# Kernel tuning notes

Hardware: AMD Instinct MI355X
Metric: run time of the kernel (lower is better)

The kernel has to match this reference:

```python
import jax, jax.numpy as jnp
import numpy as np

INPUT_SIZE = 300
HIDDEN = 128
NUM_CLASSES = 2
B, T = 256, 512


def setup_inputs() -> dict:
    key = jax.random.key(0)
    ks = jax.random.split(key, 7)
    s_ih = 1.0 / np.sqrt(HIDDEN)
    x = jax.random.normal(ks[0], (B, T, INPUT_SIZE), dtype=jnp.float32)
    W_ih = jax.random.uniform(ks[1], (HIDDEN, INPUT_SIZE), minval=-s_ih, maxval=s_ih, dtype=jnp.float32)
    W_hh = jax.random.uniform(ks[2], (HIDDEN, HIDDEN), minval=-s_ih, maxval=s_ih, dtype=jnp.float32)
    b_ih = jax.random.uniform(ks[3], (HIDDEN,), minval=-s_ih, maxval=s_ih, dtype=jnp.float32)
    b_hh = jax.random.uniform(ks[4], (HIDDEN,), minval=-s_ih, maxval=s_ih, dtype=jnp.float32)
    fc_w = jax.random.uniform(ks[5], (NUM_CLASSES, HIDDEN), minval=-s_ih, maxval=s_ih, dtype=jnp.float32)
    fc_b = jax.random.uniform(ks[6], (NUM_CLASSES,), minval=-s_ih, maxval=s_ih, dtype=jnp.float32)
    return {"x": x, "W_ih": W_ih, "W_hh": W_hh, "b_ih": b_ih, "b_hh": b_hh, "fc_w": fc_w, "fc_b": fc_b}


def reference(x, W_ih, W_hh, b_ih, b_hh, fc_w, fc_b):
    # Precompute input projections for all timesteps: [B,T,H]
    xp = jnp.einsum('bti,hi->bth', x, W_ih) + b_ih + b_hh
    h0 = jnp.zeros((x.shape[0], HIDDEN), dtype=x.dtype)

    def step(h, xp_t):  # xp_t: [B,H]
        h_new = jnp.tanh(xp_t + h @ W_hh.T)
        return h_new, None

    h_last, _ = jax.lax.scan(step, h0, jnp.swapaxes(xp, 0, 1))  # scan over T
    # Final FC on last hidden state (out[:, -1, :] of the RNN outputs)
    return h_last @ fc_w.T + fc_b
```

## Files before the change

kernel.cpp:

```cpp
#include <hip/hip_runtime.h>
#include <cstdint>
#include <cstddef>

#define KIN 300
#define KPAD 320
#define HIDDEN 128
#define BSZ 256
#define TSZ 512

typedef __attribute__((ext_vector_type(8))) short short8;
typedef __attribute__((ext_vector_type(4))) float f32x4;

__device__ __forceinline__ short f2bf(float f) {
  uint32_t u = __builtin_bit_cast(uint32_t, f);
  u = (u + 0x7FFFu + ((u >> 16) & 1u)) >> 16;
  return (short)u;
}
__device__ __forceinline__ float bf2f(short s) {
  uint32_t u = ((uint32_t)(uint16_t)s) << 16;
  return __builtin_bit_cast(float, u);
}
__device__ __forceinline__ float bflo(uint32_t u) {
  return __builtin_bit_cast(float, u << 16);
}
__device__ __forceinline__ float bfhi(uint32_t u) {
  return __builtin_bit_cast(float, u & 0xFFFF0000u);
}
__device__ __forceinline__ uint32_t pack2bf(float a, float b) {
  return (uint32_t)(uint16_t)f2bf(a) | ((uint32_t)(uint16_t)f2bf(b) << 16);
}
__device__ __forceinline__ float tanhf_fast(float v) {
  const float e = __builtin_amdgcn_exp2f(v * 2.88539008177793f);
  return fmaf(-2.0f, __builtin_amdgcn_rcpf(e + 1.0f), 1.0f);
}
__device__ __forceinline__ void barrier_lds() {
  asm volatile("s_waitcnt lgkmcnt(0)\n\ts_barrier" ::: "memory");
}
__device__ __forceinline__ void barrier_all() {
  asm volatile("s_waitcnt vmcnt(0) lgkmcnt(0)\n\ts_barrier" ::: "memory");
}
__device__ __forceinline__ void dma16(const short* g, short* l) {
  __builtin_amdgcn_global_load_lds(
      (const __attribute__((address_space(1))) void*)g,
      (__attribute__((address_space(3))) void*)l, 16, 0, 0);
}

__global__ __launch_bounds__(256) void wcvt_bf16(const float* __restrict__ W,
                                                 short* __restrict__ W16) {
  const int i = blockIdx.x * 256 + threadIdx.x;
  if (i >= HIDDEN * KPAD) return;
  const int n = i / KPAD, k = i % KPAD;
  W16[i] = (k < KIN) ? f2bf(W[n * KIN + k]) : (short)0;
}

__global__ __launch_bounds__(256) void xp_gemm_mfma(
    const float* __restrict__ x, const short* __restrict__ W16,
    const float* __restrict__ b_ih, const float* __restrict__ b_hh,
    short* __restrict__ xp16) {
  __shared__ __align__(16) short As[64 * 328];
  const int tid = threadIdx.x;
  const int lane = tid & 63, w = tid >> 6;
  const int q = lane >> 4, c = lane & 15;
  const int bg = blockIdx.x & 15, tc = blockIdx.x >> 4;
  const int b0 = bg * 16, t0 = tc * 4;

#pragma unroll
  for (int i = 0; i < 19; ++i) {
    const int f = tid + 256 * i;
    if (f < 4800) {
      const int rr = f / 75;
      const int k4 = f - rr * 75;
      const int b_in = rr >> 2, t_loc = rr & 3;
      const float4 v = *(const float4*)(
          x + ((size_t)(b0 + b_in) * TSZ + t0 + t_loc) * KIN + k4 * 4);
      uint2 pv;
      pv.x = pack2bf(v.x, v.y);
      pv.y = pack2bf(v.z, v.w);
      *(uint2*)&As[rr * 328 + k4 * 4] = pv;
    }
  }
  if (tid < 64) {
    const uint2 z = {0u, 0u};
#pragma unroll
    for (int j = 0; j < 5; ++j) *(uint2*)&As[tid * 328 + 300 + j * 4] = z;
  }
  __syncthreads();

  f32x4 acc[2][4];
#pragma unroll
  for (int ht = 0; ht < 2; ++ht)
#pragma unroll
    for (int rt = 0; rt < 4; ++rt) acc[ht][rt] = (f32x4){0.f, 0.f, 0.f, 0.f};

  const short* wp0 = W16 + (size_t)((2 * w + 0) * 16 + c) * KPAD + q * 8;
  const short* wp1 = W16 + (size_t)((2 * w + 1) * 16 + c) * KPAD + q * 8;
  short8 af[2][2];
  af[0][0] = *(const short8*)(wp0);
  af[0][1] = *(const short8*)(wp1);
#pragma unroll
  for (int kc = 0; kc < 10; ++kc) {
    const int cur = kc & 1;
    if (kc < 9) {
      af[cur ^ 1][0] = *(const short8*)(wp0 + (kc + 1) * 32);
      af[cur ^ 1][1] = *(const short8*)(wp1 + (kc + 1) * 32);
    }
    short8 bq[4];
#pragma unroll
    for (int rt = 0; rt < 4; ++rt)
      bq[rt] = *(const short8*)&As[(rt * 16 + c) * 328 + kc * 32 + q * 8];
#pragma unroll
    for (int ht = 0; ht < 2; ++ht)
#pragma unroll
      for (int rt = 0; rt < 4; ++rt)
        acc[ht][rt] = __builtin_amdgcn_mfma_f32_16x16x32_bf16(
            af[cur][ht], bq[rt], acc[ht][rt], 0, 0, 0);
  }
  __syncthreads();

  float4 bsum[2];
#pragma unroll
  for (int ht = 0; ht < 2; ++ht) {
    const int h0 = (2 * w + ht) * 16 + q * 4;
    const float4 bi = *(const float4*)(b_ih + h0);
    const float4 bh = *(const float4*)(b_hh + h0);
    bsum[ht] = make_float4(bi.x + bh.x, bi.y + bh.y, bi.z + bh.z, bi.w + bh.w);
  }
#pragma unroll
  for (int ht = 0; ht < 2; ++ht) {
    const int g = (2 * w + ht) * 4 + q;
#pragma unroll
    for (int rt = 0; rt < 4; ++rt) {
      const int b_in = rt * 4 + (c >> 2);
      const int t_loc = c & 3;
      uint2 pv;
      pv.x = pack2bf(acc[ht][rt][0] + bsum[ht].x, acc[ht][rt][1] + bsum[ht].y);
      pv.y = pack2bf(acc[ht][rt][2] + bsum[ht].z, acc[ht][rt][3] + bsum[ht].w);
      *(uint2*)&As[t_loc * 2312 + g * 72 + b_in * 4] = pv;
    }
  }
  __syncthreads();
#pragma unroll
  for (int i = 0; i < 4; ++i) {
    const int4 vv =
        *(const int4*)&As[i * 2312 + (tid >> 3) * 72 + (tid & 7) * 8];
    *(int4*)(xp16 + ((size_t)(t0 + i) * 16 + bg) * 2048 + tid * 8) = vv;
  }
}

__global__ __launch_bounds__(256, 1) void rnn_scan_dma(
    const short* __restrict__ xp16, const float* __restrict__ Whh,
    const float* __restrict__ fc_w, const float* __restrict__ fc_b,
    float* __restrict__ out) {
  __shared__ __align__(16) short xs[2][8][2048];
  __shared__ __align__(16) short ht[2][16][136];
  const int tid = threadIdx.x;
  const int lane = tid & 63, w = tid >> 6;
  const int q = lane >> 4, c = lane & 15;
  const int bg = blockIdx.x;

  short8 aw[2][4];
#pragma unroll
  for (int ti = 0; ti < 2; ++ti)
#pragma unroll
    for (int kc = 0; kc < 4; ++kc) {
      const float* src =
          Whh + (size_t)(w * 32 + ti * 16 + c) * HIDDEN + kc * 32 + q * 8;
      const float4 v0 = *(const float4*)(src);
      const float4 v1 = *(const float4*)(src + 4);
      short8 t;
      t[0] = f2bf(v0.x); t[1] = f2bf(v0.y); t[2] = f2bf(v0.z); t[3] = f2bf(v0.w);
      t[4] = f2bf(v1.x); t[5] = f2bf(v1.y); t[6] = f2bf(v1.z); t[7] = f2bf(v1.w);
      aw[ti][kc] = t;
    }

  {
    uint32_t* z = (uint32_t*)&ht[0][0][0];
    for (int i = tid; i < 1088; i += 256) z[i] = 0;
  }

#define ISSUE_CHUNK(CH, BUF)                                                  \
  {                                                                           \
    _Pragma("unroll") for (int sr = 0; sr < 2; ++sr) {                        \
      const int s = 2 * w + sr;                                               \
      const short* srcb =                                                     \
          xp16 + ((size_t)((CH)*8 + s) * 16 + bg) * 2048 + lane * 8;          \
      _Pragma("unroll") for (int j = 0; j < 4; ++j)                           \
          dma16(srcb + j * 512, &xs[BUF][s][j * 512]);                        \
    }                                                                         \
  }

  ISSUE_CHUNK(0, 0)
  barrier_all();

  const int g0 = w * 8 + q, g1 = w * 8 + 4 + q;
  const int hb0 = w * 32 + q * 4, hb1 = hb0 + 16;
  const f32x4 zero4 = {0.f, 0.f, 0.f, 0.f};

  for (int cc = 0; cc < 64; ++cc) {
    const int buf = cc & 1;
    if (cc + 1 < 64) ISSUE_CHUNK(cc + 1, buf ^ 1)
#pragma unroll
    for (int s = 0; s < 8; ++s) {
      const int rb = s & 1;
      const short8 bh0 = *(const short8*)&ht[rb][c][0 + q * 8];
      const short8 bh1 = *(const short8*)&ht[rb][c][32 + q * 8];
      const short8 bh2 = *(const short8*)&ht[rb][c][64 + q * 8];
      const short8 bh3 = *(const short8*)&ht[rb][c][96 + q * 8];
      const uint2 u0 = *(const uint2*)&xs[buf][s][g0 * 64 + c * 4];
      const uint2 u1 = *(const uint2*)&xs[buf][s][g1 * 64 + c * 4];
      f32x4 p0 = {bflo(u0.x), bfhi(u0.x), bflo(u0.y), bfhi(u0.y)};
      f32x4 p1 = {bflo(u1.x), bfhi(u1.x), bflo(u1.y), bfhi(u1.y)};
      f32x4 q0 = zero4, q1 = zero4;
      p0 = __builtin_amdgcn_mfma_f32_16x16x32_bf16(aw[0][0], bh0, p0, 0, 0, 0);
      p1 = __builtin_amdgcn_mfma_f32_16x16x32_bf16(aw[1][0], bh0, p1, 0, 0, 0);
      q0 = __builtin_amdgcn_mfma_f32_16x16x32_bf16(aw[0][1], bh1, q0, 0, 0, 0);
      q1 = __builtin_amdgcn_mfma_f32_16x16x32_bf16(aw[1][1], bh1, q1, 0, 0, 0);
      p0 = __builtin_amdgcn_mfma_f32_16x16x32_bf16(aw[0][2], bh2, p0, 0, 0, 0);
      p1 = __builtin_amdgcn_mfma_f32_16x16x32_bf16(aw[1][2], bh2, p1, 0, 0, 0);
      q0 = __builtin_amdgcn_mfma_f32_16x16x32_bf16(aw[0][3], bh3, q0, 0, 0, 0);
      q1 = __builtin_amdgcn_mfma_f32_16x16x32_bf16(aw[1][3], bh3, q1, 0, 0, 0);
      const f32x4 s0 = p0 + q0;
      const f32x4 s1 = p1 + q1;
      uint2 w0, w1;
      w0.x = pack2bf(tanhf_fast(s0[0]), tanhf_fast(s0[1]));
      w0.y = pack2bf(tanhf_fast(s0[2]), tanhf_fast(s0[3]));
      w1.x = pack2bf(tanhf_fast(s1[0]), tanhf_fast(s1[1]));
      w1.y = pack2bf(tanhf_fast(s1[2]), tanhf_fast(s1[3]));
      *(uint2*)&ht[rb ^ 1][c][hb0] = w0;
      *(uint2*)&ht[rb ^ 1][c][hb1] = w1;
      barrier_lds();
    }
    barrier_all();
  }
#undef ISSUE_CHUNK

  if (tid < 32) {
    const int bi = tid >> 1, cls = tid & 1;
    float s = fc_b[cls];
    const float* fw = fc_w + cls * HIDDEN;
#pragma unroll 8
    for (int k = 0; k < HIDDEN; k += 4) {
      s = fmaf(bf2f(ht[0][bi][k + 0]), fw[k + 0], s);
      s = fmaf(bf2f(ht[0][bi][k + 1]), fw[k + 1], s);
      s = fmaf(bf2f(ht[0][bi][k + 2]), fw[k + 2], s);
      s = fmaf(bf2f(ht[0][bi][k + 3]), fw[k + 3], s);
    }
    out[(bg * 16 + bi) * 2 + cls] = s;
  }
}

extern "C" void kernel_launch(void* const* d_in, const int* in_sizes, int n_in,
                              void* d_out, int out_size, void* d_ws, size_t ws_size,
                              hipStream_t stream) {
  const float* x    = (const float*)d_in[0];
  const float* W_ih = (const float*)d_in[1];
  const float* W_hh = (const float*)d_in[2];
  const float* b_ih = (const float*)d_in[3];
  const float* b_hh = (const float*)d_in[4];
  const float* fc_w = (const float*)d_in[5];
  const float* fc_b = (const float*)d_in[6];
  short* xp16 = (short*)d_ws;
  short* W16  = (short*)((char*)d_ws + (33u << 20));
  float* out  = (float*)d_out;

  wcvt_bf16<<<(HIDDEN * KPAD + 255) / 256, 256, 0, stream>>>(W_ih, W16);
  xp_gemm_mfma<<<16 * (TSZ / 4), 256, 0, stream>>>(x, W16, b_ih, b_hh, xp16);
  rnn_scan_dma<<<16, 256, 0, stream>>>(xp16, W_hh, fc_w, fc_b, out);
}
```

Baseline: 509.7 us.

## Split recurrent scan across 8 waves, one 16-row hidden tile each

The recurrent scan block grows from 4 to 8 wavefronts. Each wave now owns a single 16-row slice of the hidden state and issues 4 MFMAs per step instead of 8, which shortens the serial per-timestep critical path. Each wave also DMAs one timestep slice per chunk and loads all 8 xp values up front. The cost is a block-wide barrier across twice as many waves at every timestep, which may offset the shorter MFMA chain.

New measurement: 448.5 us. 1.14x faster.

```diff
diff --git a/kernel.cpp b/kernel.cpp
--- a/kernel.cpp
+++ b/kernel.cpp
@@ -147,7 +147,7 @@
   }
 }
 
-__global__ __launch_bounds__(256, 1) void rnn_scan_dma(
+__global__ __launch_bounds__(512, 2) void rnn_scan_dma(
     const short* __restrict__ xp16, const float* __restrict__ Whh,
     const float* __restrict__ fc_w, const float* __restrict__ fc_b,
     float* __restrict__ out) {
@@ -158,47 +158,44 @@
   const int q = lane >> 4, c = lane & 15;
   const int bg = blockIdx.x;
 
-  short8 aw[2][4];
-#pragma unroll
-  for (int ti = 0; ti < 2; ++ti)
-#pragma unroll
-    for (int kc = 0; kc < 4; ++kc) {
-      const float* src =
-          Whh + (size_t)(w * 32 + ti * 16 + c) * HIDDEN + kc * 32 + q * 8;
-      const float4 v0 = *(const float4*)(src);
-      const float4 v1 = *(const float4*)(src + 4);
-      short8 t;
-      t[0] = f2bf(v0.x); t[1] = f2bf(v0.y); t[2] = f2bf(v0.z); t[3] = f2bf(v0.w);
-      t[4] = f2bf(v1.x); t[5] = f2bf(v1.y); t[6] = f2bf(v1.z); t[7] = f2bf(v1.w);
-      aw[ti][kc] = t;
-    }
+  short8 aw[4];
+#pragma unroll
+  for (int kc = 0; kc < 4; ++kc) {
+    const float* src = Whh + (size_t)(w * 16 + c) * HIDDEN + kc * 32 + q * 8;
+    const float4 v0 = *(const float4*)(src);
+    const float4 v1 = *(const float4*)(src + 4);
+    short8 t;
+    t[0] = f2bf(v0.x); t[1] = f2bf(v0.y); t[2] = f2bf(v0.z); t[3] = f2bf(v0.w);
+    t[4] = f2bf(v1.x); t[5] = f2bf(v1.y); t[6] = f2bf(v1.z); t[7] = f2bf(v1.w);
+    aw[kc] = t;
+  }
 
   {
     uint32_t* z = (uint32_t*)&ht[0][0][0];
-    for (int i = tid; i < 1088; i += 256) z[i] = 0;
+    for (int i = tid; i < 1088; i += 512) z[i] = 0;
   }
 
 #define ISSUE_CHUNK(CH, BUF)                                                  \
   {                                                                           \
-    _Pragma("unroll") for (int sr = 0; sr < 2; ++sr) {                        \
-      const int s = 2 * w + sr;                                               \
-      const short* srcb =                                                     \
-          xp16 + ((size_t)((CH)*8 + s) * 16 + bg) * 2048 + lane * 8;          \
-      _Pragma("unroll") for (int j = 0; j < 4; ++j)                           \
-          dma16(srcb + j * 512, &xs[BUF][s][j * 512]);                        \
-    }                                                                         \
+    const short* srcb =                                                       \
+        xp16 + ((size_t)((CH)*8 + w) * 16 + bg) * 2048 + lane * 8;            \
+    _Pragma("unroll") for (int j = 0; j < 4; ++j)                             \
+        dma16(srcb + j * 512, &xs[BUF][w][j * 512]);                          \
   }
 
   ISSUE_CHUNK(0, 0)
   barrier_all();
 
-  const int g0 = w * 8 + q, g1 = w * 8 + 4 + q;
-  const int hb0 = w * 32 + q * 4, hb1 = hb0 + 16;
+  const int gx = (w * 4 + q) * 64 + c * 4;
+  const int hb = w * 16 + q * 4;
   const f32x4 zero4 = {0.f, 0.f, 0.f, 0.f};
 
   for (int cc = 0; cc < 64; ++cc) {
     const int buf = cc & 1;
     if (cc + 1 < 64) ISSUE_CHUNK(cc + 1, buf ^ 1)
+    uint2 us[8];
+#pragma unroll
+    for (int s = 0; s < 8; ++s) us[s] = *(const uint2*)&xs[buf][s][gx];
 #pragma unroll
     for (int s = 0; s < 8; ++s) {
       const int rb = s & 1;
@@ -206,28 +203,17 @@
       const short8 bh1 = *(const short8*)&ht[rb][c][32 + q * 8];
       const short8 bh2 = *(const short8*)&ht[rb][c][64 + q * 8];
       const short8 bh3 = *(const short8*)&ht[rb][c][96 + q * 8];
-      const uint2 u0 = *(const uint2*)&xs[buf][s][g0 * 64 + c * 4];
-      const uint2 u1 = *(const uint2*)&xs[buf][s][g1 * 64 + c * 4];
-      f32x4 p0 = {bflo(u0.x), bfhi(u0.x), bflo(u0.y), bfhi(u0.y)};
-      f32x4 p1 = {bflo(u1.x), bfhi(u1.x), bflo(u1.y), bfhi(u1.y)};
-      f32x4 q0 = zero4, q1 = zero4;
-      p0 = __builtin_amdgcn_mfma_f32_16x16x32_bf16(aw[0][0], bh0, p0, 0, 0, 0);
-      p1 = __builtin_amdgcn_mfma_f32_16x16x32_bf16(aw[1][0], bh0, p1, 0, 0, 0);
-      q0 = __builtin_amdgcn_mfma_f32_16x16x32_bf16(aw[0][1], bh1, q0, 0, 0, 0);
-      q1 = __builtin_amdgcn_mfma_f32_16x16x32_bf16(aw[1][1], bh1, q1, 0, 0, 0);
-      p0 = __builtin_amdgcn_mfma_f32_16x16x32_bf16(aw[0][2], bh2, p0, 0, 0, 0);
-      p1 = __builtin_amdgcn_mfma_f32_16x16x32_bf16(aw[1][2], bh2, p1, 0, 0, 0);
-      q0 = __builtin_amdgcn_mfma_f32_16x16x32_bf16(aw[0][3], bh3, q0, 0, 0, 0);
-      q1 = __builtin_amdgcn_mfma_f32_16x16x32_bf16(aw[1][3], bh3, q1, 0, 0, 0);
-      const f32x4 s0 = p0 + q0;
-      const f32x4 s1 = p1 + q1;
-      uint2 w0, w1;
+      f32x4 a0 = {bflo(us[s].x), bfhi(us[s].x), bflo(us[s].y), bfhi(us[s].y)};
+      f32x4 a1 = zero4, a2 = zero4, a3 = zero4;
+      a0 = __builtin_amdgcn_mfma_f32_16x16x32_bf16(aw[0], bh0, a0, 0, 0, 0);
+      a1 = __builtin_amdgcn_mfma_f32_16x16x32_bf16(aw[1], bh1, a1, 0, 0, 0);
+      a2 = __builtin_amdgcn_mfma_f32_16x16x32_bf16(aw[2], bh2, a2, 0, 0, 0);
+      a3 = __builtin_amdgcn_mfma_f32_16x16x32_bf16(aw[3], bh3, a3, 0, 0, 0);
+      const f32x4 s0 = (a0 + a1) + (a2 + a3);
+      uint2 w0;
       w0.x = pack2bf(tanhf_fast(s0[0]), tanhf_fast(s0[1]));
       w0.y = pack2bf(tanhf_fast(s0[2]), tanhf_fast(s0[3]));
-      w1.x = pack2bf(tanhf_fast(s1[0]), tanhf_fast(s1[1]));
-      w1.y = pack2bf(tanhf_fast(s1[2]), tanhf_fast(s1[3]));
-      *(uint2*)&ht[rb ^ 1][c][hb0] = w0;
-      *(uint2*)&ht[rb ^ 1][c][hb1] = w1;
+      *(uint2*)&ht[rb ^ 1][c][hb] = w0;
       barrier_lds();
     }
     barrier_all();
@@ -265,5 +251,5 @@
 
   wcvt_bf16<<<(HIDDEN * KPAD + 255) / 256, 256, 0, stream>>>(W_ih, W16);
   xp_gemm_mfma<<<16 * (TSZ / 4), 256, 0, stream>>>(x, W16, b_ih, b_hh, xp16);
-  rnn_scan_dma<<<16, 256, 0, stream>>>(xp16, W_hh, fc_w, fc_b, out);
-}
+  rnn_scan_dma<<<16, 512, 0, stream>>>(xp16, W_hh, fc_w, fc_b, out);
+}
```

## Interleave xp layout for single 16B loads, prefetch LDS operands, use hw bf16 pack

Applied to the files above, without the earlier changes.

Changes the xp16 staging layout so each scan lane gets both M-tiles' input projections in one 16-byte LDS load, and hoists all eight per-step loads to the start of each chunk. It also double-buffers the B-operand LDS reads in the projection GEMM, pads the LDS row stride, reorders the MFMA chains, and swaps the software bf16 rounding in pack2bf for the v_cvt_pk_bf16_f32 instruction. The goal is fewer LDS instructions and less latency on the serial recurrence critical path, at the cost of more registers held per chunk. The zeroing loop now writes the whole ht buffer, both halves.

New measurement: 455.5 us. -10.6%, faster.

```diff
diff --git a/kernel.cpp b/kernel.cpp
--- a/kernel.cpp
+++ b/kernel.cpp
@@ -8,7 +8,12 @@
 #define BSZ 256
 #define TSZ 512
 
+#define ASTR 332
+#define ST1 2176
+#define HSTR 136
+
 typedef __attribute__((ext_vector_type(8))) short short8;
+typedef __attribute__((ext_vector_type(4))) short s16x4;
 typedef __attribute__((ext_vector_type(4))) float f32x4;
 
 __device__ __forceinline__ short f2bf(float f) {
@@ -27,7 +32,9 @@
   return __builtin_bit_cast(float, u & 0xFFFF0000u);
 }
 __device__ __forceinline__ uint32_t pack2bf(float a, float b) {
-  return (uint32_t)(uint16_t)f2bf(a) | ((uint32_t)(uint16_t)f2bf(b) << 16);
+  uint32_t r;
+  asm("v_cvt_pk_bf16_f32 %0, %1, %2" : "=v"(r) : "v"(a), "v"(b));
+  return r;
 }
 __device__ __forceinline__ float tanhf_fast(float v) {
   const float e = __builtin_amdgcn_exp2f(v * 2.88539008177793f);
@@ -57,7 +64,7 @@
     const float* __restrict__ x, const short* __restrict__ W16,
     const float* __restrict__ b_ih, const float* __restrict__ b_hh,
     short* __restrict__ xp16) {
-  __shared__ __align__(16) short As[64 * 328];
+  __shared__ __align__(16) short As[64 * ASTR];
   const int tid = threadIdx.x;
   const int lane = tid & 63, w = tid >> 6;
   const int q = lane >> 4, c = lane & 15;
@@ -76,13 +83,13 @@
       uint2 pv;
       pv.x = pack2bf(v.x, v.y);
       pv.y = pack2bf(v.z, v.w);
-      *(uint2*)&As[rr * 328 + k4 * 4] = pv;
+      *(uint2*)&As[rr * ASTR + k4 * 4] = pv;
     }
   }
   if (tid < 64) {
     const uint2 z = {0u, 0u};
 #pragma unroll
-    for (int j = 0; j < 5; ++j) *(uint2*)&As[tid * 328 + 300 + j * 4] = z;
+    for (int j = 0; j < 5; ++j) *(uint2*)&As[tid * ASTR + 300 + j * 4] = z;
   }
   __syncthreads();
 
@@ -94,26 +101,30 @@
 
   const short* wp0 = W16 + (size_t)((2 * w + 0) * 16 + c) * KPAD + q * 8;
   const short* wp1 = W16 + (size_t)((2 * w + 1) * 16 + c) * KPAD + q * 8;
+  const short* bqp = &As[c * ASTR + q * 8];
   short8 af[2][2];
+  short8 bq[2][4];
   af[0][0] = *(const short8*)(wp0);
   af[0][1] = *(const short8*)(wp1);
+#pragma unroll
+  for (int rt = 0; rt < 4; ++rt)
+    bq[0][rt] = *(const short8*)(bqp + rt * 16 * ASTR);
 #pragma unroll
   for (int kc = 0; kc < 10; ++kc) {
     const int cur = kc & 1;
     if (kc < 9) {
       af[cur ^ 1][0] = *(const short8*)(wp0 + (kc + 1) * 32);
       af[cur ^ 1][1] = *(const short8*)(wp1 + (kc + 1) * 32);
-    }
-    short8 bq[4];
-#pragma unroll
-    for (int rt = 0; rt < 4; ++rt)
-      bq[rt] = *(const short8*)&As[(rt * 16 + c) * 328 + kc * 32 + q * 8];
+#pragma unroll
+      for (int rt = 0; rt < 4; ++rt)
+        bq[cur ^ 1][rt] = *(const short8*)(bqp + rt * 16 * ASTR + (kc + 1) * 32);
+    }
 #pragma unroll
     for (int ht = 0; ht < 2; ++ht)
 #pragma unroll
       for (int rt = 0; rt < 4; ++rt)
         acc[ht][rt] = __builtin_amdgcn_mfma_f32_16x16x32_bf16(
-            af[cur][ht], bq[rt], acc[ht][rt], 0, 0, 0);
+            af[cur][ht], bq[cur][rt], acc[ht][rt], 0, 0, 0);
   }
   __syncthreads();
 
@@ -128,6 +139,8 @@
 #pragma unroll
   for (int ht = 0; ht < 2; ++ht) {
     const int g = (2 * w + ht) * 4 + q;
+    const int u = 4 * (g >> 3) + (g & 3);
+    const int mt = (g >> 2) & 1;
 #pragma unroll
     for (int rt = 0; rt < 4; ++rt) {
       const int b_in = rt * 4 + (c >> 2);
@@ -135,14 +148,14 @@
       uint2 pv;
       pv.x = pack2bf(acc[ht][rt][0] + bsum[ht].x, acc[ht][rt][1] + bsum[ht].y);
       pv.y = pack2bf(acc[ht][rt][2] + bsum[ht].z, acc[ht][rt][3] + bsum[ht].w);
-      *(uint2*)&As[t_loc * 2312 + g * 72 + b_in * 4] = pv;
+      *(uint2*)&As[t_loc * ST1 + u * 136 + b_in * 8 + mt * 4] = pv;
     }
   }
   __syncthreads();
 #pragma unroll
   for (int i = 0; i < 4; ++i) {
     const int4 vv =
-        *(const int4*)&As[i * 2312 + (tid >> 3) * 72 + (tid & 7) * 8];
+        *(const int4*)&As[i * ST1 + (tid >> 4) * 136 + (tid & 15) * 8];
     *(int4*)(xp16 + ((size_t)(t0 + i) * 16 + bg) * 2048 + tid * 8) = vv;
   }
 }
@@ -152,7 +165,7 @@
     const float* __restrict__ fc_w, const float* __restrict__ fc_b,
     float* __restrict__ out) {
   __shared__ __align__(16) short xs[2][8][2048];
-  __shared__ __align__(16) short ht[2][16][136];
+  __shared__ __align__(16) short ht[2][16][HSTR];
   const int tid = threadIdx.x;
   const int lane = tid & 63, w = tid >> 6;
   const int q = lane >> 4, c = lane & 15;
@@ -160,22 +173,22 @@
 
   short8 aw[2][4];
 #pragma unroll
-  for (int ti = 0; ti < 2; ++ti)
+  for (int mt = 0; mt < 2; ++mt)
 #pragma unroll
     for (int kc = 0; kc < 4; ++kc) {
       const float* src =
-          Whh + (size_t)(w * 32 + ti * 16 + c) * HIDDEN + kc * 32 + q * 8;
+          Whh + (size_t)(32 * w + 16 * mt + c) * HIDDEN + kc * 32 + q * 8;
       const float4 v0 = *(const float4*)(src);
       const float4 v1 = *(const float4*)(src + 4);
       short8 t;
       t[0] = f2bf(v0.x); t[1] = f2bf(v0.y); t[2] = f2bf(v0.z); t[3] = f2bf(v0.w);
       t[4] = f2bf(v1.x); t[5] = f2bf(v1.y); t[6] = f2bf(v1.z); t[7] = f2bf(v1.w);
-      aw[ti][kc] = t;
+      aw[mt][kc] = t;
     }
 
   {
     uint32_t* z = (uint32_t*)&ht[0][0][0];
-    for (int i = tid; i < 1088; i += 256) z[i] = 0;
+    for (int i = tid; i < 2176; i += 256) z[i] = 0;
   }
 
 #define ISSUE_CHUNK(CH, BUF)                                                  \
@@ -192,42 +205,43 @@
   ISSUE_CHUNK(0, 0)
   barrier_all();
 
-  const int g0 = w * 8 + q, g1 = w * 8 + 4 + q;
-  const int hb0 = w * 32 + q * 4, hb1 = hb0 + 16;
+  const int xsoff = (4 * w + q) * 128 + c * 8;
   const f32x4 zero4 = {0.f, 0.f, 0.f, 0.f};
 
   for (int cc = 0; cc < 64; ++cc) {
     const int buf = cc & 1;
     if (cc + 1 < 64) ISSUE_CHUNK(cc + 1, buf ^ 1)
+    uint4 us[8];
+#pragma unroll
+    for (int s = 0; s < 8; ++s) us[s] = *(const uint4*)&xs[buf][s][xsoff];
 #pragma unroll
     for (int s = 0; s < 8; ++s) {
       const int rb = s & 1;
-      const short8 bh0 = *(const short8*)&ht[rb][c][0 + q * 8];
-      const short8 bh1 = *(const short8*)&ht[rb][c][32 + q * 8];
-      const short8 bh2 = *(const short8*)&ht[rb][c][64 + q * 8];
-      const short8 bh3 = *(const short8*)&ht[rb][c][96 + q * 8];
-      const uint2 u0 = *(const uint2*)&xs[buf][s][g0 * 64 + c * 4];
-      const uint2 u1 = *(const uint2*)&xs[buf][s][g1 * 64 + c * 4];
-      f32x4 p0 = {bflo(u0.x), bfhi(u0.x), bflo(u0.y), bfhi(u0.y)};
-      f32x4 p1 = {bflo(u1.x), bfhi(u1.x), bflo(u1.y), bfhi(u1.y)};
-      f32x4 q0 = zero4, q1 = zero4;
+      const short* bp = &ht[rb][c][q * 8];
+      const short8 bh0 = *(const short8*)(bp + 0);
+      const short8 bh1 = *(const short8*)(bp + 32);
+      const short8 bh2 = *(const short8*)(bp + 64);
+      const short8 bh3 = *(const short8*)(bp + 96);
+      f32x4 p0 = {bflo(us[s].x), bfhi(us[s].x), bflo(us[s].y), bfhi(us[s].y)};
+      f32x4 p1 = {bflo(us[s].z), bfhi(us[s].z), bflo(us[s].w), bfhi(us[s].w)};
+      f32x4 r0 = zero4, r1 = zero4;
       p0 = __builtin_amdgcn_mfma_f32_16x16x32_bf16(aw[0][0], bh0, p0, 0, 0, 0);
+      r0 = __builtin_amdgcn_mfma_f32_16x16x32_bf16(aw[0][2], bh2, r0, 0, 0, 0);
       p1 = __builtin_amdgcn_mfma_f32_16x16x32_bf16(aw[1][0], bh0, p1, 0, 0, 0);
-      q0 = __builtin_amdgcn_mfma_f32_16x16x32_bf16(aw[0][1], bh1, q0, 0, 0, 0);
-      q1 = __builtin_amdgcn_mfma_f32_16x16x32_bf16(aw[1][1], bh1, q1, 0, 0, 0);
-      p0 = __builtin_amdgcn_mfma_f32_16x16x32_bf16(aw[0][2], bh2, p0, 0, 0, 0);
-      p1 = __builtin_amdgcn_mfma_f32_16x16x32_bf16(aw[1][2], bh2, p1, 0, 0, 0);
-      q0 = __builtin_amdgcn_mfma_f32_16x16x32_bf16(aw[0][3], bh3, q0, 0, 0, 0);
-      q1 = __builtin_amdgcn_mfma_f32_16x16x32_bf16(aw[1][3], bh3, q1, 0, 0, 0);
-      const f32x4 s0 = p0 + q0;
-      const f32x4 s1 = p1 + q1;
+      r1 = __builtin_amdgcn_mfma_f32_16x16x32_bf16(aw[1][2], bh2, r1, 0, 0, 0);
+      p0 = __builtin_amdgcn_mfma_f32_16x16x32_bf16(aw[0][1], bh1, p0, 0, 0, 0);
+      r0 = __builtin_amdgcn_mfma_f32_16x16x32_bf16(aw[0][3], bh3, r0, 0, 0, 0);
+      p1 = __builtin_amdgcn_mfma_f32_16x16x32_bf16(aw[1][1], bh1, p1, 0, 0, 0);
+      r1 = __builtin_amdgcn_mfma_f32_16x16x32_bf16(aw[1][3], bh3, r1, 0, 0, 0);
+      const f32x4 s0 = p0 + r0;
+      const f32x4 s1 = p1 + r1;
       uint2 w0, w1;
       w0.x = pack2bf(tanhf_fast(s0[0]), tanhf_fast(s0[1]));
       w0.y = pack2bf(tanhf_fast(s0[2]), tanhf_fast(s0[3]));
       w1.x = pack2bf(tanhf_fast(s1[0]), tanhf_fast(s1[1]));
       w1.y = pack2bf(tanhf_fast(s1[2]), tanhf_fast(s1[3]));
-      *(uint2*)&ht[rb ^ 1][c][hb0] = w0;
-      *(uint2*)&ht[rb ^ 1][c][hb1] = w1;
+      *(uint2*)&ht[rb ^ 1][c][32 * w + 4 * q] = w0;
+      *(uint2*)&ht[rb ^ 1][c][32 * w + 16 + 4 * q] = w1;
       barrier_lds();
     }
     barrier_all();
```
